# Optimization experiments

Hardware: AMD Instinct MI355X
Metric: run time of the kernel (lower is better)

Reference implementation:

```python
import jax, jax.numpy as jnp
import numpy as np

HIDDEN = 1024
N_HEADS = 16
HEAD_DIM = HIDDEN // N_HEADS


def setup_inputs() -> dict:
    key = jax.random.key(0)
    ks = jax.random.split(key, 7)
    b, l, m = 4, 1024, 1024
    q = jax.random.normal(ks[0], (b, l, HIDDEN), dtype=jnp.float32)
    k = jax.random.normal(ks[1], (b, m, HIDDEN), dtype=jnp.float32)
    v = jax.random.normal(ks[2], (b, m, HIDDEN), dtype=jnp.float32)
    s = 1.0 / np.sqrt(HIDDEN)
    w_q = jax.random.normal(ks[3], (HIDDEN, HIDDEN), dtype=jnp.float32) * s
    w_k = jax.random.normal(ks[4], (HIDDEN, HIDDEN), dtype=jnp.float32) * s
    w_v = jax.random.normal(ks[5], (HIDDEN, HIDDEN), dtype=jnp.float32) * s
    w_o = jax.random.normal(ks[6], (HIDDEN, HIDDEN), dtype=jnp.float32) * s
    return {"q": q, "k": k, "v": v, "w_q": w_q, "w_k": w_k, "w_v": w_v, "w_o": w_o}


def reference(q, k, v, w_q, w_k, w_v, w_o):
    b, l, _ = q.shape
    _, m, _ = k.shape
    # Linear (bias=False): y = x @ W^T
    qp = q @ w_q.T
    kp = k @ w_k.T
    vp = v @ w_v.T  # projected but unused downstream (faithful to original bug)
    # Faithful non-standard split: hidden -> (head_dim, n_heads)
    qh = qp.reshape(b, l, HEAD_DIM, N_HEADS)
    kh = kp.reshape(b, m, HEAD_DIM, N_HEADS)
    # attn over K, scaled, softmax over m (dim=2)
    scores = jnp.einsum('bldn,bmdn->blmn', qh, kh) / np.sqrt(HEAD_DIM)
    attn = jax.nn.softmax(scores, axis=2)
    # dropout is identity in eval mode
    # NOTE: original attends over K (not V) — reproduced faithfully
    x = jnp.einsum('blmn,bmdn->bldn', attn, kh)
    x = x.reshape(b, l, HIDDEN)  # 'b l d n -> b l (d n)'
    return x @ w_o.T
```

## Files before the change

### kernel.cpp

```cpp
#include <hip/hip_runtime.h>
#include <hip/hip_bf16.h>
#include <stdint.h>
#include <math.h>


typedef __bf16 bf16;
typedef __bf16 bf16x8 __attribute__((ext_vector_type(8)));
typedef float  f32x4  __attribute__((ext_vector_type(4)));

__device__ __forceinline__ void async_load16(const void* g, void* l) {
  __builtin_amdgcn_global_load_lds((__attribute__((address_space(1))) void*)g,
                                   (__attribute__((address_space(3))) void*)l,
                                   16, 0, 0);
}

__device__ __forceinline__ float load_canon(const void* src, int i, int fl) {
  float f = fl ? ((const float*)src)[i] : (float)((const bf16*)src)[i];
  return fminf(fmaxf(f, -1024.f), 1024.f);
}

__global__ void __launch_bounds__(256)
canon_all(const void* __restrict__ q_raw, const void* __restrict__ k_raw,
          const void* __restrict__ wq_raw, const void* __restrict__ wk_raw,
          const void* __restrict__ wo_raw,
          bf16* __restrict__ q_c, bf16* __restrict__ k_c,
          bf16* __restrict__ wq_c, bf16* __restrict__ wk_c,
          bf16* __restrict__ wo_p, int* __restrict__ flag) {
  __shared__ int smax[4];
  const int tid = threadIdx.x;
  {
    int e = (((const unsigned short*)q_raw)[tid] >> 7) & 0xFF;
#pragma unroll
    for (int off = 1; off <= 32; off <<= 1) {
      int o = __shfl_xor(e, off);
      e = o > e ? o : e;
    }
    if ((tid & 63) == 0) smax[tid >> 6] = e;
  }
  __syncthreads();
  int m01 = smax[0] > smax[1] ? smax[0] : smax[1];
  int m23 = smax[2] > smax[3] ? smax[2] : smax[3];
  const int fl = ((m01 > m23 ? m01 : m23) >= 140) ? 1 : 0;

  const int blk = blockIdx.x;
  if (blk == 0 && tid == 0) *flag = fl;

  if (blk < 4096) {
    const void* src = blk < 2048 ? q_raw : k_raw;
    bf16* dst = blk < 2048 ? q_c : k_c;
    int i = (blk & 2047) * 2048 + tid * 8;
    bf16x8 v;
#pragma unroll
    for (int j = 0; j < 8; ++j) v[j] = (bf16)load_canon(src, i + j, fl);
    *(bf16x8*)(dst + i) = v;
  } else if (blk < 5120) {
    const void* src = blk < 4608 ? wq_raw : wk_raw;
    bf16* dst = blk < 4608 ? wq_c : wk_c;
    int i = ((blk - 4096) & 511) * 2048 + tid * 8;
    bf16x8 v;
#pragma unroll
    for (int j = 0; j < 8; ++j) v[j] = (bf16)load_canon(src, i + j, fl);
    *(bf16x8*)(dst + i) = v;
  } else {
    int i = (blk - 5120) * 2048 + tid * 8;
    int o = i >> 10, h0 = i & 1023;
#pragma unroll
    for (int j = 0; j < 8; ++j) {
      int h = h0 + j;
      int kp = ((h & 15) << 6) | (h >> 4);
      wo_p[o * 1024 + kp] = (bf16)load_canon(wo_raw, i + j, fl);
    }
  }
}

__global__ void __launch_bounds__(256, 2)
qk_gemm(const bf16* __restrict__ q_c, const bf16* __restrict__ wq_c,
        const bf16* __restrict__ k_c, const bf16* __restrict__ wk_c,
        bf16* __restrict__ qh, bf16* __restrict__ kh, bf16* __restrict__ khT,
        float cs) {
  __shared__ bf16 sA[128 * 64];
  __shared__ bf16 sB[128 * 64];
  __shared__ bf16 epi[128 * 134];

  const int z = blockIdx.z;
  const bf16* A = z ? k_c : q_c;
  const bf16* W = z ? wk_c : wq_c;
  const float scale = z ? 1.0f : cs;
  bf16* out0 = z ? kh : qh;

  const int tid  = threadIdx.x;
  const int lane = tid & 63;
  const int wave = tid >> 6;
  const int q4   = lane >> 4;
  const int c16  = lane & 15;
  const int wm   = wave >> 1;
  const int wn   = wave & 1;

  const int lin    = blockIdx.x + 8 * blockIdx.y;
  const int rowBlk = (lin & 31) * 128;
  const int colBlk = (lin >> 5) * 128;

  int ar[4], ag[4];
#pragma unroll
  for (int i = 0; i < 4; ++i) {
    int s = tid + 256 * i;
    ar[i] = s >> 3;
    ag[i] = (tid & 7) ^ (ar[i] & 7);
  }
  const bf16* gA[4];
  const bf16* gB[4];
  bf16 *lA[4], *lB[4];
#pragma unroll
  for (int i = 0; i < 4; ++i) {
    gA[i] = A + (size_t)(rowBlk + ar[i]) * 1024 + ag[i] * 8;
    gB[i] = W + (size_t)(colBlk + ar[i]) * 1024 + ag[i] * 8;
    lA[i] = sA + (tid + 256 * i) * 8;
    lB[i] = sB + (tid + 256 * i) * 8;
  }

  f32x4 acc[4][4] = {};

  for (int kk = 0; kk < 1024; kk += 64) {
    __syncthreads();
#pragma unroll
    for (int i = 0; i < 4; ++i) async_load16(gA[i] + kk, lA[i]);
#pragma unroll
    for (int i = 0; i < 4; ++i) async_load16(gB[i] + kk, lB[i]);
    __builtin_amdgcn_s_waitcnt(0);
    __syncthreads();

    bf16x8 af[2][4], bfr[2][4];
#pragma unroll
    for (int ks = 0; ks < 2; ++ks) {
#pragma unroll
      for (int mt = 0; mt < 4; ++mt) {
        int row = wm * 64 + mt * 16 + c16;
        af[ks][mt] = *(const bf16x8*)(sA + row * 64 +
                       (((ks * 4 + q4) ^ (row & 7)) * 8));
      }
#pragma unroll
      for (int nt = 0; nt < 4; ++nt) {
        int row = wn * 64 + nt * 16 + c16;
        bfr[ks][nt] = *(const bf16x8*)(sB + row * 64 +
                       (((ks * 4 + q4) ^ (row & 7)) * 8));
      }
    }
#pragma unroll
    for (int ks = 0; ks < 2; ++ks)
#pragma unroll
      for (int mt = 0; mt < 4; ++mt)
#pragma unroll
        for (int nt = 0; nt < 4; ++nt)
          acc[mt][nt] = __builtin_amdgcn_mfma_f32_16x16x32_bf16(
              af[ks][mt], bfr[ks][nt], acc[mt][nt], 0, 0, 0);
  }

  __syncthreads();
#pragma unroll
  for (int mt = 0; mt < 4; ++mt)
#pragma unroll
    for (int nt = 0; nt < 4; ++nt)
#pragma unroll
      for (int r = 0; r < 4; ++r) {
        int m_t = wm * 64 + mt * 16 + q4 * 4 + r;
        int h_t = wn * 64 + nt * 16 + c16;
        epi[m_t * 134 + h_t] = (bf16)(acc[mt][nt][r] * scale);
      }
  __syncthreads();

  const int bb    = rowBlk >> 10;
  const int mbase = rowBlk & 1023;
  const int dg0   = colBlk >> 4;

  {
    int n = tid >> 4;
#pragma unroll
    for (int i = 0; i < 8; ++i) {
      int m_t = (tid & 15) + i * 16;
      bf16x8 v;
#pragma unroll
      for (int dt = 0; dt < 8; ++dt) v[dt] = epi[m_t * 134 + dt * 16 + n];
      *(bf16x8*)(out0 + ((size_t)(bb * 16 + n) * 1024 + mbase + m_t) * 64 + dg0) = v;
    }
  }
  if (z) {
    int h_t = tid >> 1, half = tid & 1;
    int n = h_t & 15, dt = h_t >> 4;
    size_t base = ((size_t)(bb * 16 + n) * 64 + dg0 + dt) * 1024 + mbase + half * 64;
#pragma unroll
    for (int c = 0; c < 8; ++c) {
      bf16x8 v;
#pragma unroll
      for (int j = 0; j < 8; ++j) v[j] = epi[(half * 64 + c * 8 + j) * 134 + h_t];
      *(bf16x8*)(khT + base + c * 8) = v;
    }
  }
}

__global__ void __launch_bounds__(256, 2)
o_gemm(const bf16* __restrict__ A, const bf16* __restrict__ W,
       bf16* __restrict__ out0, float* __restrict__ outf,
       const int* __restrict__ flag) {
  __shared__ bf16 sA[128 * 64];
  __shared__ bf16 sB[64 * 64];

  const int tid  = threadIdx.x;
  const int lane = tid & 63;
  const int wave = tid >> 6;
  const int q4   = lane >> 4;
  const int c16  = lane & 15;
  const int wm   = wave >> 1;
  const int wn   = wave & 1;

  const int lin    = blockIdx.x + 16 * blockIdx.y;
  const int rowBlk = (lin & 31) * 128;
  const int colBlk = (lin >> 5) * 64;

  int ar[4], ag[4];
#pragma unroll
  for (int i = 0; i < 4; ++i) {
    int s = tid + 256 * i;
    ar[i] = s >> 3;
    ag[i] = (tid & 7) ^ (ar[i] & 7);
  }
  const bf16* gA[4];
  bf16* lA[4];
#pragma unroll
  for (int i = 0; i < 4; ++i) {
    gA[i] = A + (size_t)(rowBlk + ar[i]) * 1024 + ag[i] * 8;
    lA[i] = sA + (tid + 256 * i) * 8;
  }
  const bf16* gB[2];
  bf16* lB[2];
#pragma unroll
  for (int i = 0; i < 2; ++i) {
    int s = tid + 256 * i;
    int br = s >> 3, bg = (tid & 7) ^ (br & 7);
    gB[i] = W + (size_t)(colBlk + br) * 1024 + bg * 8;
    lB[i] = sB + s * 8;
  }

  f32x4 acc[4][2] = {};

  for (int kk = 0; kk < 1024; kk += 64) {
    __syncthreads();
#pragma unroll
    for (int i = 0; i < 4; ++i) async_load16(gA[i] + kk, lA[i]);
#pragma unroll
    for (int i = 0; i < 2; ++i) async_load16(gB[i] + kk, lB[i]);
    __builtin_amdgcn_s_waitcnt(0);
    __syncthreads();

    bf16x8 af[2][4], bfr[2][2];
#pragma unroll
    for (int ks = 0; ks < 2; ++ks) {
#pragma unroll
      for (int mt = 0; mt < 4; ++mt) {
        int row = wm * 64 + mt * 16 + c16;
        af[ks][mt] = *(const bf16x8*)(sA + row * 64 +
                       (((ks * 4 + q4) ^ (row & 7)) * 8));
      }
#pragma unroll
      for (int nt = 0; nt < 2; ++nt) {
        int row = wn * 32 + nt * 16 + c16;
        bfr[ks][nt] = *(const bf16x8*)(sB + row * 64 +
                       (((ks * 4 + q4) ^ (row & 7)) * 8));
      }
    }
#pragma unroll
    for (int ks = 0; ks < 2; ++ks)
#pragma unroll
      for (int mt = 0; mt < 4; ++mt)
#pragma unroll
        for (int nt = 0; nt < 2; ++nt)
          acc[mt][nt] = __builtin_amdgcn_mfma_f32_16x16x32_bf16(
              af[ks][mt], bfr[ks][nt], acc[mt][nt], 0, 0, 0);
  }

  const int fl = *flag;
#pragma unroll
  for (int mt = 0; mt < 4; ++mt)
#pragma unroll
    for (int nt = 0; nt < 2; ++nt)
#pragma unroll
      for (int r = 0; r < 4; ++r) {
        int gm = rowBlk + wm * 64 + mt * 16 + q4 * 4 + r;
        int gn = colBlk + wn * 32 + nt * 16 + c16;
        size_t idx = (size_t)gm * 1024 + gn;
        if (fl) outf[idx] = acc[mt][nt][r];
        else    out0[idx] = (bf16)acc[mt][nt][r];
      }
}

__global__ void __launch_bounds__(256, 2)
attn_kernel(const bf16* __restrict__ qh, const bf16* __restrict__ kh,
            const bf16* __restrict__ khT, bf16* __restrict__ xh) {
  __shared__ bf16 sK[64 * 64];
  __shared__ bf16 sKT[64 * 64];
  __shared__ bf16 sP[4][32 * 72];

  const int tid  = threadIdx.x;
  const int lane = tid & 63;
  const int wave = tid >> 6;
  const int q4   = lane >> 4;
  const int c16  = lane & 15;
  const int bn   = blockIdx.x;
  const int b    = bn >> 4, n = bn & 15;
  const int l0w  = blockIdx.y * 128 + wave * 32;

  const bf16* qhead  = qh  + (size_t)bn * (1024 * 64);
  const bf16* khead  = kh  + (size_t)bn * (1024 * 64);
  const bf16* kThead = khT + (size_t)bn * (64 * 1024);

  bf16x8 aq[2][2];
#pragma unroll
  for (int g = 0; g < 2; ++g)
#pragma unroll
    for (int hh = 0; hh < 2; ++hh)
      aq[g][hh] = *(const bf16x8*)(qhead +
                    (size_t)(l0w + g * 16 + c16) * 64 + hh * 32 + q4 * 8);

  const int s0 = tid, s1 = tid + 256;
  const int r0 = s0 >> 3, g0 = (s0 & 7) ^ (r0 & 7);
  const int r1 = s1 >> 3, g1 = (s1 & 7) ^ (r1 & 7);

  f32x4 O[2][4] = {};
  f32x4 Osum[2] = {};
  bf16x8 ones;
#pragma unroll
  for (int j = 0; j < 8; ++j) ones[j] = (bf16)1.0f;
  bf16* sPw = sP[wave];

  for (int m0 = 0; m0 < 1024; m0 += 64) {
    __syncthreads();
    async_load16(khead + (size_t)(m0 + r0) * 64 + g0 * 8, sK + s0 * 8);
    async_load16(khead + (size_t)(m0 + r1) * 64 + g1 * 8, sK + s1 * 8);
    async_load16(kThead + (size_t)r0 * 1024 + m0 + g0 * 8, sKT + s0 * 8);
    async_load16(kThead + (size_t)r1 * 1024 + m0 + g1 * 8, sKT + s1 * 8);
    __builtin_amdgcn_s_waitcnt(0);
    __syncthreads();

    f32x4 S[2][4] = {};
#pragma unroll
    for (int t = 0; t < 4; ++t) {
#pragma unroll
      for (int hh = 0; hh < 2; ++hh) {
        int row = t * 16 + c16;
        bf16x8 bk = *(const bf16x8*)(sK + row * 64 +
                                     (((hh * 4 + q4) ^ (row & 7)) * 8));
        S[0][t] = __builtin_amdgcn_mfma_f32_16x16x32_bf16(aq[0][hh], bk, S[0][t], 0, 0, 0);
        S[1][t] = __builtin_amdgcn_mfma_f32_16x16x32_bf16(aq[1][hh], bk, S[1][t], 0, 0, 0);
      }
    }

#pragma unroll
    for (int g = 0; g < 2; ++g)
#pragma unroll
      for (int t = 0; t < 4; ++t)
#pragma unroll
        for (int r = 0; r < 4; ++r) {
          float p = __builtin_amdgcn_exp2f(S[g][t][r]);
          sPw[(g * 16 + q4 * 4 + r) * 72 + t * 16 + c16] = (bf16)p;
        }

    bf16x8 ap[2][2];
#pragma unroll
    for (int g = 0; g < 2; ++g) {
      ap[g][0] = *(const bf16x8*)(sPw + (g * 16 + c16) * 72 + q4 * 8);
      ap[g][1] = *(const bf16x8*)(sPw + (g * 16 + c16) * 72 + 32 + q4 * 8);
      Osum[g] = __builtin_amdgcn_mfma_f32_16x16x32_bf16(ap[g][0], ones, Osum[g], 0, 0, 0);
      Osum[g] = __builtin_amdgcn_mfma_f32_16x16x32_bf16(ap[g][1], ones, Osum[g], 0, 0, 0);
    }

#pragma unroll
    for (int td = 0; td < 4; ++td) {
#pragma unroll
      for (int hh = 0; hh < 2; ++hh) {
        int row = td * 16 + c16;
        bf16x8 bkt = *(const bf16x8*)(sKT + row * 64 +
                                      (((hh * 4 + q4) ^ (row & 7)) * 8));
        O[0][td] = __builtin_amdgcn_mfma_f32_16x16x32_bf16(ap[0][hh], bkt, O[0][td], 0, 0, 0);
        O[1][td] = __builtin_amdgcn_mfma_f32_16x16x32_bf16(ap[1][hh], bkt, O[1][td], 0, 0, 0);
      }
    }
  }

#pragma unroll
  for (int g = 0; g < 2; ++g) {
    float inv[4];
#pragma unroll
    for (int r = 0; r < 4; ++r) inv[r] = 1.0f / Osum[g][r];
#pragma unroll
    for (int td = 0; td < 4; ++td)
#pragma unroll
      for (int r = 0; r < 4; ++r)
        sPw[(g * 16 + q4 * 4 + r) * 72 + td * 16 + c16] = (bf16)(O[g][td][r] * inv[r]);
  }
  {
    int l_loc = lane >> 2, dq = lane & 3;
#pragma unroll
    for (int g = 0; g < 2; ++g) {
      bf16x8 v0 = *(const bf16x8*)(sPw + (g * 16 + l_loc) * 72 + dq * 16);
      bf16x8 v1 = *(const bf16x8*)(sPw + (g * 16 + l_loc) * 72 + dq * 16 + 8);
      size_t base = ((size_t)(b * 1024 + l0w + g * 16 + l_loc) * 16 + n) * 64 + dq * 16;
      *(bf16x8*)(xh + base)     = v0;
      *(bf16x8*)(xh + base + 8) = v1;
    }
  }
}

extern "C" void kernel_launch(void* const* d_in, const int* in_sizes, int n_in,
                              void* d_out, int out_size, void* d_ws, size_t ws_size,
                              hipStream_t stream) {
  const void* q_raw  = d_in[0];
  const void* k_raw  = d_in[1];
  const void* wq_raw = d_in[3];
  const void* wk_raw = d_in[4];
  const void* wo_raw = d_in[6];

  char* ws = (char*)d_ws;
  const size_t MB = 1024 * 1024;
  bf16* q_c  = (bf16*)(ws + 0 * MB);
  bf16* xh   = (bf16*)(ws + 0 * MB);
  bf16* k_c  = (bf16*)(ws + 8 * MB);
  bf16* kh   = (bf16*)(ws + 16 * MB);
  bf16* wq_c = (bf16*)(ws + 24 * MB);
  bf16* wk_c = (bf16*)(ws + 26 * MB);
  bf16* wo_p = (bf16*)(ws + 28 * MB);
  int*  flag = (int*)(ws + 30 * MB);
  bf16* qh   = (bf16*)d_out;
  bf16* khT  = (bf16*)((char*)d_out + 8 * MB);

  const float CS = 0.125f * 1.4426950408889634f;
  dim3 blk(256, 1, 1);

  hipLaunchKernelGGL(canon_all, dim3(5632), blk, 0, stream,
                     q_raw, k_raw, wq_raw, wk_raw, wo_raw,
                     q_c, k_c, wq_c, wk_c, wo_p, flag);
  hipLaunchKernelGGL(qk_gemm, dim3(8, 32, 2), blk, 0, stream,
                     q_c, wq_c, k_c, wk_c, qh, kh, khT, CS);
  hipLaunchKernelGGL(attn_kernel, dim3(64, 8, 1), blk, 0, stream,
                     qh, kh, khT, xh);
  hipLaunchKernelGGL(o_gemm, dim3(16, 32, 1), blk, 0, stream,
                     xh, wo_p, (bf16*)d_out, (float*)d_out, flag);
}
```

Before: 191.8 us.

## Double K-tile depth to 128 in GEMMs and attention, vectorize w_o permute

After: 191.9 us. No clear change (+0.1%).

```diff
diff --git a/kernel.cpp b/kernel.cpp
--- a/kernel.cpp
+++ b/kernel.cpp
@@ -62,14 +62,16 @@
     for (int j = 0; j < 8; ++j) v[j] = (bf16)load_canon(src, i + j, fl);
     *(bf16x8*)(dst + i) = v;
   } else {
-    int i = (blk - 5120) * 2048 + tid * 8;
-    int o = i >> 10, h0 = i & 1023;
+    int d0 = (blk - 5120) * 2048 + tid * 8;
+    int o = d0 >> 10, kp0 = d0 & 1023;
+    bf16x8 v;
 #pragma unroll
     for (int j = 0; j < 8; ++j) {
-      int h = h0 + j;
-      int kp = ((h & 15) << 6) | (h >> 4);
-      wo_p[o * 1024 + kp] = (bf16)load_canon(wo_raw, i + j, fl);
-    }
+      int kp = kp0 + j;
+      int h = ((kp & 63) << 4) | (kp >> 6);
+      v[j] = (bf16)load_canon(wo_raw, o * 1024 + h, fl);
+    }
+    *(bf16x8*)(wo_p + d0) = v;
   }
 }
 
@@ -78,9 +80,10 @@
         const bf16* __restrict__ k_c, const bf16* __restrict__ wk_c,
         bf16* __restrict__ qh, bf16* __restrict__ kh, bf16* __restrict__ khT,
         float cs) {
-  __shared__ bf16 sA[128 * 64];
-  __shared__ bf16 sB[128 * 64];
-  __shared__ bf16 epi[128 * 134];
+  __shared__ __attribute__((aligned(16))) char smem[64 * 1024];
+  bf16* sA  = (bf16*)smem;
+  bf16* sB  = (bf16*)(smem + 32 * 1024);
+  bf16* epi = (bf16*)smem;
 
   const int z = blockIdx.z;
   const bf16* A = z ? k_c : q_c;
@@ -100,18 +103,18 @@
   const int rowBlk = (lin & 31) * 128;
   const int colBlk = (lin >> 5) * 128;
 
-  int ar[4], ag[4];
-#pragma unroll
-  for (int i = 0; i < 4; ++i) {
+  int ar[8], ag[8];
+#pragma unroll
+  for (int i = 0; i < 8; ++i) {
     int s = tid + 256 * i;
-    ar[i] = s >> 3;
-    ag[i] = (tid & 7) ^ (ar[i] & 7);
-  }
-  const bf16* gA[4];
-  const bf16* gB[4];
-  bf16 *lA[4], *lB[4];
-#pragma unroll
-  for (int i = 0; i < 4; ++i) {
+    ar[i] = s >> 4;
+    ag[i] = (s & 15) ^ (ar[i] & 15);
+  }
+  const bf16* gA[8];
+  const bf16* gB[8];
+  bf16 *lA[8], *lB[8];
+#pragma unroll
+  for (int i = 0; i < 8; ++i) {
     gA[i] = A + (size_t)(rowBlk + ar[i]) * 1024 + ag[i] * 8;
     gB[i] = W + (size_t)(colBlk + ar[i]) * 1024 + ag[i] * 8;
     lA[i] = sA + (tid + 256 * i) * 8;
@@ -120,39 +123,37 @@
 
   f32x4 acc[4][4] = {};
 
-  for (int kk = 0; kk < 1024; kk += 64) {
-    __syncthreads();
-#pragma unroll
-    for (int i = 0; i < 4; ++i) async_load16(gA[i] + kk, lA[i]);
-#pragma unroll
-    for (int i = 0; i < 4; ++i) async_load16(gB[i] + kk, lB[i]);
+  for (int kk = 0; kk < 1024; kk += 128) {
+    __syncthreads();
+#pragma unroll
+    for (int i = 0; i < 8; ++i) async_load16(gA[i] + kk, lA[i]);
+#pragma unroll
+    for (int i = 0; i < 8; ++i) async_load16(gB[i] + kk, lB[i]);
     __builtin_amdgcn_s_waitcnt(0);
     __syncthreads();
 
-    bf16x8 af[2][4], bfr[2][4];
-#pragma unroll
-    for (int ks = 0; ks < 2; ++ks) {
+#pragma unroll
+    for (int ks = 0; ks < 4; ++ks) {
+      bf16x8 af[4], bfr[4];
 #pragma unroll
       for (int mt = 0; mt < 4; ++mt) {
         int row = wm * 64 + mt * 16 + c16;
-        af[ks][mt] = *(const bf16x8*)(sA + row * 64 +
-                       (((ks * 4 + q4) ^ (row & 7)) * 8));
+        af[mt] = *(const bf16x8*)(sA + row * 128 +
+                   (((ks * 4 + q4) ^ (row & 15)) * 8));
       }
 #pragma unroll
       for (int nt = 0; nt < 4; ++nt) {
         int row = wn * 64 + nt * 16 + c16;
-        bfr[ks][nt] = *(const bf16x8*)(sB + row * 64 +
-                       (((ks * 4 + q4) ^ (row & 7)) * 8));
-      }
-    }
-#pragma unroll
-    for (int ks = 0; ks < 2; ++ks)
+        bfr[nt] = *(const bf16x8*)(sB + row * 128 +
+                   (((ks * 4 + q4) ^ (row & 15)) * 8));
+      }
 #pragma unroll
       for (int mt = 0; mt < 4; ++mt)
 #pragma unroll
         for (int nt = 0; nt < 4; ++nt)
           acc[mt][nt] = __builtin_amdgcn_mfma_f32_16x16x32_bf16(
-              af[ks][mt], bfr[ks][nt], acc[mt][nt], 0, 0, 0);
+              af[mt], bfr[nt], acc[mt][nt], 0, 0, 0);
+    }
   }
 
   __syncthreads();
@@ -201,8 +202,8 @@
 o_gemm(const bf16* __restrict__ A, const bf16* __restrict__ W,
        bf16* __restrict__ out0, float* __restrict__ outf,
        const int* __restrict__ flag) {
-  __shared__ bf16 sA[128 * 64];
-  __shared__ bf16 sB[64 * 64];
+  __shared__ bf16 sA[128 * 128];
+  __shared__ bf16 sB[64 * 128];
 
   const int tid  = threadIdx.x;
   const int lane = tid & 63;
@@ -216,65 +217,63 @@
   const int rowBlk = (lin & 31) * 128;
   const int colBlk = (lin >> 5) * 64;
 
-  int ar[4], ag[4];
+  int ar[8], ag[8];
+#pragma unroll
+  for (int i = 0; i < 8; ++i) {
+    int s = tid + 256 * i;
+    ar[i] = s >> 4;
+    ag[i] = (s & 15) ^ (ar[i] & 15);
+  }
+  const bf16* gA[8];
+  bf16* lA[8];
+#pragma unroll
+  for (int i = 0; i < 8; ++i) {
+    gA[i] = A + (size_t)(rowBlk + ar[i]) * 1024 + ag[i] * 8;
+    lA[i] = sA + (tid + 256 * i) * 8;
+  }
+  const bf16* gB[4];
+  bf16* lB[4];
 #pragma unroll
   for (int i = 0; i < 4; ++i) {
     int s = tid + 256 * i;
-    ar[i] = s >> 3;
-    ag[i] = (tid & 7) ^ (ar[i] & 7);
-  }
-  const bf16* gA[4];
-  bf16* lA[4];
-#pragma unroll
-  for (int i = 0; i < 4; ++i) {
-    gA[i] = A + (size_t)(rowBlk + ar[i]) * 1024 + ag[i] * 8;
-    lA[i] = sA + (tid + 256 * i) * 8;
-  }
-  const bf16* gB[2];
-  bf16* lB[2];
-#pragma unroll
-  for (int i = 0; i < 2; ++i) {
-    int s = tid + 256 * i;
-    int br = s >> 3, bg = (tid & 7) ^ (br & 7);
+    int br = s >> 4, bg = (s & 15) ^ (br & 15);
     gB[i] = W + (size_t)(colBlk + br) * 1024 + bg * 8;
     lB[i] = sB + s * 8;
   }
 
   f32x4 acc[4][2] = {};
 
-  for (int kk = 0; kk < 1024; kk += 64) {
-    __syncthreads();
-#pragma unroll
-    for (int i = 0; i < 4; ++i) async_load16(gA[i] + kk, lA[i]);
-#pragma unroll
-    for (int i = 0; i < 2; ++i) async_load16(gB[i] + kk, lB[i]);
+  for (int kk = 0; kk < 1024; kk += 128) {
+    __syncthreads();
+#pragma unroll
+    for (int i = 0; i < 8; ++i) async_load16(gA[i] + kk, lA[i]);
+#pragma unroll
+    for (int i = 0; i < 4; ++i) async_load16(gB[i] + kk, lB[i]);
     __builtin_amdgcn_s_waitcnt(0);
     __syncthreads();
 
-    bf16x8 af[2][4], bfr[2][2];
-#pragma unroll
-    for (int ks = 0; ks < 2; ++ks) {
+#pragma unroll
+    for (int ks = 0; ks < 4; ++ks) {
+      bf16x8 af[4], bfr[2];
 #pragma unroll
       for (int mt = 0; mt < 4; ++mt) {
         int row = wm * 64 + mt * 16 + c16;
-        af[ks][mt] = *(const bf16x8*)(sA + row * 64 +
-                       (((ks * 4 + q4) ^ (row & 7)) * 8));
+        af[mt] = *(const bf16x8*)(sA + row * 128 +
+                   (((ks * 4 + q4) ^ (row & 15)) * 8));
       }
 #pragma unroll
       for (int nt = 0; nt < 2; ++nt) {
         int row = wn * 32 + nt * 16 + c16;
-        bfr[ks][nt] = *(const bf16x8*)(sB + row * 64 +
-                       (((ks * 4 + q4) ^ (row & 7)) * 8));
-      }
-    }
-#pragma unroll
-    for (int ks = 0; ks < 2; ++ks)
+        bfr[nt] = *(const bf16x8*)(sB + row * 128 +
+                   (((ks * 4 + q4) ^ (row & 15)) * 8));
+      }
 #pragma unroll
       for (int mt = 0; mt < 4; ++mt)
 #pragma unroll
         for (int nt = 0; nt < 2; ++nt)
           acc[mt][nt] = __builtin_amdgcn_mfma_f32_16x16x32_bf16(
-              af[ks][mt], bfr[ks][nt], acc[mt][nt], 0, 0, 0);
+              af[mt], bfr[nt], acc[mt][nt], 0, 0, 0);
+    }
   }
 
   const int fl = *flag;
@@ -295,9 +294,9 @@
 __global__ void __launch_bounds__(256, 2)
 attn_kernel(const bf16* __restrict__ qh, const bf16* __restrict__ kh,
             const bf16* __restrict__ khT, bf16* __restrict__ xh) {
-  __shared__ bf16 sK[64 * 64];
-  __shared__ bf16 sKT[64 * 64];
-  __shared__ bf16 sP[4][32 * 72];
+  __shared__ bf16 sK[128 * 64];
+  __shared__ bf16 sKT[64 * 128];
+  __shared__ bf16 sP[4][32 * 136];
 
   const int tid  = threadIdx.x;
   const int lane = tid & 63;
@@ -320,9 +319,13 @@
       aq[g][hh] = *(const bf16x8*)(qhead +
                     (size_t)(l0w + g * 16 + c16) * 64 + hh * 32 + q4 * 8);
 
-  const int s0 = tid, s1 = tid + 256;
-  const int r0 = s0 >> 3, g0 = (s0 & 7) ^ (r0 & 7);
-  const int r1 = s1 >> 3, g1 = (s1 & 7) ^ (r1 & 7);
+  int kr[4], kg[4], tr[4], tg[4];
+#pragma unroll
+  for (int i = 0; i < 4; ++i) {
+    int s = tid + 256 * i;
+    kr[i] = s >> 3;  kg[i] = (s & 7) ^ (kr[i] & 7);
+    tr[i] = s >> 4;  tg[i] = (s & 15) ^ (tr[i] & 15);
+  }
 
   f32x4 O[2][4] = {};
   f32x4 Osum[2] = {};
@@ -331,18 +334,21 @@
   for (int j = 0; j < 8; ++j) ones[j] = (bf16)1.0f;
   bf16* sPw = sP[wave];
 
-  for (int m0 = 0; m0 < 1024; m0 += 64) {
-    __syncthreads();
-    async_load16(khead + (size_t)(m0 + r0) * 64 + g0 * 8, sK + s0 * 8);
-    async_load16(khead + (size_t)(m0 + r1) * 64 + g1 * 8, sK + s1 * 8);
-    async_load16(kThead + (size_t)r0 * 1024 + m0 + g0 * 8, sKT + s0 * 8);
-    async_load16(kThead + (size_t)r1 * 1024 + m0 + g1 * 8, sKT + s1 * 8);
+  for (int m0 = 0; m0 < 1024; m0 += 128) {
+    __syncthreads();
+#pragma unroll
+    for (int i = 0; i < 4; ++i) {
+      async_load16(khead + (size_t)(m0 + kr[i]) * 64 + kg[i] * 8,
+                   sK + (tid + 256 * i) * 8);
+      async_load16(kThead + (size_t)tr[i] * 1024 + m0 + tg[i] * 8,
+                   sKT + (tid + 256 * i) * 8);
+    }
     __builtin_amdgcn_s_waitcnt(0);
     __syncthreads();
 
-    f32x4 S[2][4] = {};
-#pragma unroll
-    for (int t = 0; t < 4; ++t) {
+    f32x4 S[2][8] = {};
+#pragma unroll
+    for (int t = 0; t < 8; ++t) {
 #pragma unroll
       for (int hh = 0; hh < 2; ++hh) {
         int row = t * 16 + c16;
@@ -356,31 +362,33 @@
 #pragma unroll
     for (int g = 0; g < 2; ++g)
 #pragma unroll
-      for (int t = 0; t < 4; ++t)
+      for (int t = 0; t < 8; ++t)
 #pragma unroll
         for (int r = 0; r < 4; ++r) {
           float p = __builtin_amdgcn_exp2f(S[g][t][r]);
-          sPw[(g * 16 + q4 * 4 + r) * 72 + t * 16 + c16] = (bf16)p;
+          sPw[(g * 16 + q4 * 4 + r) * 136 + t * 16 + c16] = (bf16)p;
         }
 
-    bf16x8 ap[2][2];
+    bf16x8 ap[2][4];
 #pragma unroll
     for (int g = 0; g < 2; ++g) {
-      ap[g][0] = *(const bf16x8*)(sPw + (g * 16 + c16) * 72 + q4 * 8);
-      ap[g][1] = *(const bf16x8*)(sPw + (g * 16 + c16) * 72 + 32 + q4 * 8);
-      Osum[g] = __builtin_amdgcn_mfma_f32_16x16x32_bf16(ap[g][0], ones, Osum[g], 0, 0, 0);
-      Osum[g] = __builtin_amdgcn_mfma_f32_16x16x32_bf16(ap[g][1], ones, Osum[g], 0, 0, 0);
+#pragma unroll
+      for (int kk2 = 0; kk2 < 4; ++kk2) {
+        ap[g][kk2] = *(const bf16x8*)(sPw + (g * 16 + c16) * 136 +
+                                      kk2 * 32 + q4 * 8);
+        Osum[g] = __builtin_amdgcn_mfma_f32_16x16x32_bf16(ap[g][kk2], ones, Osum[g], 0, 0, 0);
+      }
     }
 
 #pragma unroll
     for (int td = 0; td < 4; ++td) {
 #pragma unroll
-      for (int hh = 0; hh < 2; ++hh) {
+      for (int kk2 = 0; kk2 < 4; ++kk2) {
         int row = td * 16 + c16;
-        bf16x8 bkt = *(const bf16x8*)(sKT + row * 64 +
-                                      (((hh * 4 + q4) ^ (row & 7)) * 8));
-        O[0][td] = __builtin_amdgcn_mfma_f32_16x16x32_bf16(ap[0][hh], bkt, O[0][td], 0, 0, 0);
-        O[1][td] = __builtin_amdgcn_mfma_f32_16x16x32_bf16(ap[1][hh], bkt, O[1][td], 0, 0, 0);
+        bf16x8 bkt = *(const bf16x8*)(sKT + row * 128 +
+                                      (((kk2 * 4 + q4) ^ (row & 15)) * 8));
+        O[0][td] = __builtin_amdgcn_mfma_f32_16x16x32_bf16(ap[0][kk2], bkt, O[0][td], 0, 0, 0);
+        O[1][td] = __builtin_amdgcn_mfma_f32_16x16x32_bf16(ap[1][kk2], bkt, O[1][td], 0, 0, 0);
       }
     }
   }
@@ -394,14 +402,14 @@
     for (int td = 0; td < 4; ++td)
 #pragma unroll
       for (int r = 0; r < 4; ++r)
-        sPw[(g * 16 + q4 * 4 + r) * 72 + td * 16 + c16] = (bf16)(O[g][td][r] * inv[r]);
+        sPw[(g * 16 + q4 * 4 + r) * 136 + td * 16 + c16] = (bf16)(O[g][td][r] * inv[r]);
   }
   {
     int l_loc = lane >> 2, dq = lane & 3;
 #pragma unroll
     for (int g = 0; g < 2; ++g) {
-      bf16x8 v0 = *(const bf16x8*)(sPw + (g * 16 + l_loc) * 72 + dq * 16);
-      bf16x8 v1 = *(const bf16x8*)(sPw + (g * 16 + l_loc) * 72 + dq * 16 + 8);
+      bf16x8 v0 = *(const bf16x8*)(sPw + (g * 16 + l_loc) * 136 + dq * 16);
+      bf16x8 v1 = *(const bf16x8*)(sPw + (g * 16 + l_loc) * 136 + dq * 16 + 8);
       size_t base = ((size_t)(b * 1024 + l0w + g * 16 + l_loc) * 16 + n) * 64 + dq * 16;
       *(bf16x8*)(xh + base)     = v0;
       *(bf16x8*)(xh + base + 8) = v1;
```
